# Performance work log

Measured on AMD Instinct MI355X. Metric: run time of the kernel, lower is better.

## Reference

```python
import jax, jax.numpy as jnp
import numpy as np

# ---- fixed wavelet filters (Selesnick FSfarras first-stage + Kingsbury Q-shift) ----
_F1 = np.array([
    [0.0, 0.0],
    [-0.08838834764832, -0.01122679215254],
    [0.08838834764832, 0.01122679215254],
    [0.69587998903400, 0.08838834764832],
    [0.69587998903400, 0.08838834764832],
    [0.08838834764832, -0.69587998903400],
    [-0.08838834764832, 0.69587998903400],
    [0.01122679215254, -0.08838834764832],
    [0.01122679215254, -0.08838834764832],
    [0.0, 0.0]], np.float32)
_F2 = np.array([
    [0.01122679215254, 0.0],
    [0.01122679215254, 0.0],
    [-0.08838834764832, -0.08838834764832],
    [0.08838834764832, -0.08838834764832],
    [0.69587998903400, 0.69587998903400],
    [0.69587998903400, -0.69587998903400],
    [0.08838834764832, 0.08838834764832],
    [-0.08838834764832, 0.08838834764832],
    [0.0, 0.01122679215254],
    [0.0, -0.01122679215254]], np.float32)
_Q1 = np.array([
    [0.03516384, 0.0],
    [0.0, 0.0],
    [-0.08832942, -0.11430184],
    [0.23389032, 0.0],
    [0.76027237, 0.58751830],
    [0.58751830, -0.76027237],
    [0.0, 0.23389032],
    [-0.11430184, 0.08832942],
    [0.0, 0.0],
    [0.0, -0.03516384]], np.float32)
_Q2 = np.array([
    [0.0, -0.03516384],
    [0.0, 0.0],
    [-0.11430184, 0.08832942],
    [0.0, 0.23389032],
    [0.58751830, -0.76027237],
    [0.76027237, 0.58751830],
    [0.23389032, 0.0],
    [-0.08832942, -0.11430184],
    [0.0, 0.0],
    [0.03516384, 0.0]], np.float32)
# synthesis filters are the time-reversed analysis filters
FSF = jnp.asarray(np.stack([_F1[::-1].copy(), _F2[::-1].copy()]))  # [2, 10, 2] first stage
SF = jnp.asarray(np.stack([_Q1[::-1].copy(), _Q2[::-1].copy()]))   # [2, 10, 2] Q-shift


def _upconv(x, f, axis):
    """Upsample-by-2 + full convolution with 1D filter f along `axis` (upfirdn(x,f,2,1))."""
    L = f.shape[0]
    xm = jnp.moveaxis(x, axis, -1)
    shp = xm.shape
    xr = xm.reshape(-1, 1, shp[-1])  # [M, 1, n] NCW
    k = f[::-1].astype(x.dtype).reshape(1, 1, L)  # flip -> true convolution
    y = jax.lax.conv_general_dilated(
        xr, k, window_strides=(1,), padding=[(L - 1, L - 1)],
        lhs_dilation=(2,), dimension_numbers=('NCW', 'OIW', 'NCW'))  # [M,1,2n+L-2]
    y = y.reshape(shp[:-1] + (y.shape[-1],))
    return jnp.moveaxis(y, -1, axis)


def sfb1d(lo, hi, sf, axis):
    """1D synthesis filter bank with periodic wrap + circular shift (Selesnick sfb1D)."""
    L = sf.shape[0]
    N = 2 * lo.shape[axis]
    y = _upconv(lo, sf[:, 0], axis) + _upconv(hi, sf[:, 1], axis)  # length N+L-2
    yN = jax.lax.slice_in_dim(y, 0, N, axis=axis)
    tail = jax.lax.slice_in_dim(y, N, N + L - 2, axis=axis)
    head = jax.lax.slice_in_dim(yN, 0, L - 2, axis=axis) + tail
    rest = jax.lax.slice_in_dim(yN, L - 2, N, axis=axis)
    return jnp.roll(jnp.concatenate([head, rest], axis=axis), 1 - L // 2, axis=axis)


def sfb2d(lo, hi3, sf_row, sf_col):
    """2D separable synthesis: hi3 = (LH, HL, HH); x is [B, H, W, C]."""
    lo = sfb1d(lo, hi3[0], sf_col, axis=2)
    h = sfb1d(hi3[1], hi3[2], sf_col, axis=2)
    return sfb1d(lo, h, sf_row, axis=1)


def _idtcwt(highs0, highs1, lows):
    inv_sqrt2 = jnp.asarray(1.0 / np.sqrt(2.0), highs0.dtype)

    def pm(a, b):
        return (a + b) * inv_sqrt2, (a - b) * inv_sqrt2

    # orientation butterflies per level (add_sub)
    wi = [[[[None] * 3 for _ in range(2)] for _ in range(2)] for _ in range(2)]
    for j, hj in enumerate((highs0, highs1)):
        for b in range(3):
            u, v = pm(hj[0, 0, b], hj[1, 1, b])
            wi[j][0][0][b], wi[j][1][1][b] = u, v
            u, v = pm(hj[0, 1, b], hj[1, 0, b])
            wi[j][0][1][b], wi[j][1][0][b] = u, v

    y = jnp.zeros_like(lows[0, 0], shape=(lows.shape[2], lows.shape[3] * 4,
                                          lows.shape[4] * 4, lows.shape[5]))
    for m in range(2):
        for n in range(2):
            lo = lows[m, n]
            lo = sfb2d(lo, wi[1][m][n], SF[m], SF[n])      # level 2 (Q-shift)
            lo = sfb2d(lo, wi[0][m][n], FSF[m], FSF[n])    # level 1 (first stage)
            y = y + lo
    return y / 2


def setup_inputs() -> dict:
    key = jax.random.key(0)
    k0, k1, k2 = jax.random.split(key, 3)
    B, C = 16, 3
    highs0 = jax.random.normal(k0, (2, 2, 3, B, 256, 256, C), dtype=jnp.float32)
    highs1 = jax.random.normal(k1, (2, 2, 3, B, 128, 128, C), dtype=jnp.float32)
    lows = jax.random.normal(k2, (2, 2, B, 128, 128, C), dtype=jnp.float32)
    return {"highs0": highs0, "highs1": highs1, "lows": lows}


def reference(highs0, highs1, lows):
    return _idtcwt(highs0, highs1, lows)
```

## Files before the change

### kernel.cpp

```cpp
#include <hip/hip_runtime.h>

#define INV_SQRT2 0.70710678118654752440f
#define KH 0.35355339059327376220f

constexpr float c_first[2][10][2] = {
  { { 0.00000000000000f,  0.00000000000000f},
    {-0.08838834764832f, -0.01122679215254f},
    { 0.08838834764832f,  0.01122679215254f},
    { 0.69587998903400f,  0.08838834764832f},
    { 0.69587998903400f,  0.08838834764832f},
    { 0.08838834764832f, -0.69587998903400f},
    {-0.08838834764832f,  0.69587998903400f},
    { 0.01122679215254f, -0.08838834764832f},
    { 0.01122679215254f, -0.08838834764832f},
    { 0.00000000000000f,  0.00000000000000f} },
  { { 0.01122679215254f,  0.00000000000000f},
    { 0.01122679215254f,  0.00000000000000f},
    {-0.08838834764832f, -0.08838834764832f},
    { 0.08838834764832f, -0.08838834764832f},
    { 0.69587998903400f,  0.69587998903400f},
    { 0.69587998903400f, -0.69587998903400f},
    { 0.08838834764832f,  0.08838834764832f},
    {-0.08838834764832f,  0.08838834764832f},
    { 0.00000000000000f,  0.01122679215254f},
    { 0.00000000000000f, -0.01122679215254f} }
};

constexpr float cq[2][10][2] = {
  { { 0.03516384f,  0.00000000f},
    { 0.00000000f,  0.00000000f},
    {-0.08832942f, -0.11430184f},
    { 0.23389032f,  0.00000000f},
    { 0.76027237f,  0.58751830f},
    { 0.58751830f, -0.76027237f},
    { 0.00000000f,  0.23389032f},
    {-0.11430184f,  0.08832942f},
    { 0.00000000f,  0.00000000f},
    { 0.00000000f, -0.03516384f} },
  { { 0.00000000f, -0.03516384f},
    { 0.00000000f,  0.00000000f},
    {-0.11430184f,  0.08832942f},
    { 0.00000000f,  0.23389032f},
    { 0.58751830f, -0.76027237f},
    { 0.76027237f,  0.58751830f},
    { 0.23389032f,  0.00000000f},
    {-0.08832942f, -0.11430184f},
    { 0.00000000f,  0.00000000f},
    { 0.03516384f,  0.00000000f} }
};

template<int M, int N>
__device__ __forceinline__ void s1_body(
    const float* __restrict__ lows, const float* __restrict__ highs1,
    float* __restrict__ lo2)
{
  constexpr int HIN = 128, WIN = 128, C = 3, B = 16;
  constexpr int ROWF  = WIN * C;
  constexpr int ROWO  = 2 * WIN * C;
  constexpr int PLANE = HIN * WIN * C;
  constexpr int SEG   = 16;
  constexpr int combo = M * 2 + N;
  constexpr int pa = (M == N) ? 0 : 1;
  constexpr int pb = (M == N) ? 3 : 2;
  constexpr float K = INV_SQRT2;

  const int jj = blockIdx.x * 128 + threadIdx.x;
  const int c  = jj % 3;
  const int t  = jj / 3;
  const int b  = blockIdx.z & 15;

  const float* lo = lows + (combo * B + b) * PLANE;
  const int bandStride = B * PLANE;
  const float* hA = highs1 + (pa * 3 * B + b) * PLANE;
  const float* hB = highs1 + (pb * 3 * B + b) * PLANE;

  int wc3[5];
#pragma unroll
  for (int p = 0; p < 5; ++p) {
    int w = t + 2 - p;
    if (w >= WIN) w -= WIN;
    if (w < 0)  w += WIN;
    wc3[p] = w * C + c;
  }

  float lae[5], lao[5], hae[5], hao[5];
#pragma unroll
  for (int k = 0; k < 5; ++k) { lae[k]=0.f; lao[k]=0.f; hae[k]=0.f; hao[k]=0.f; }

  const int s0 = blockIdx.y * SEG;
  float* outp = lo2 + (combo * B + b) * (4 * PLANE);

#pragma unroll 1
  for (int ui = 0; ui < SEG + 4; ++ui) {
    const int u  = (s0 - 2 + ui) & (HIN - 1);
#pragma unroll
    for (int k = 0; k < 4; ++k) { lae[k]=lae[k+1]; lao[k]=lao[k+1]; hae[k]=hae[k+1]; hao[k]=hao[k+1]; }
    const int rb = u * ROWF;

    float rl[5], rA[3][5], rB[3][5];
#pragma unroll
    for (int p = 0; p < 5; ++p) {
      const int idx = rb + wc3[p];
      rl[p]    = lo[idx];
      rA[0][p] = hA[idx];
      rB[0][p] = hB[idx];
      rA[1][p] = hA[idx +   bandStride];
      rB[1][p] = hB[idx +   bandStride];
      rA[2][p] = hA[idx + 2*bandStride];
      rB[2][p] = hB[idx + 2*bandStride];
    }
    asm volatile("" :: "v"(rl[0]),"v"(rl[1]),"v"(rl[2]),"v"(rl[3]),"v"(rl[4]),
                       "v"(rA[0][0]),"v"(rA[0][1]),"v"(rA[0][2]),"v"(rA[0][3]),"v"(rA[0][4]),
                       "v"(rA[1][0]),"v"(rA[1][1]),"v"(rA[1][2]),"v"(rA[1][3]),"v"(rA[1][4]));
    asm volatile("" :: "v"(rA[2][0]),"v"(rA[2][1]),"v"(rA[2][2]),"v"(rA[2][3]),"v"(rA[2][4]),
                       "v"(rB[0][0]),"v"(rB[0][1]),"v"(rB[0][2]),"v"(rB[0][3]),"v"(rB[0][4]),
                       "v"(rB[1][0]),"v"(rB[1][1]),"v"(rB[1][2]),"v"(rB[1][3]),"v"(rB[1][4]));
    asm volatile("" :: "v"(rB[2][0]),"v"(rB[2][1]),"v"(rB[2][2]),"v"(rB[2][3]),"v"(rB[2][4]));

    float aLe=0.f, aLo=0.f, aHe=0.f, aHo=0.f;
#pragma unroll
    for (int p = 0; p < 5; ++p) {
      const float lv  = rl[p];
      const float lhv = (M == 0) ? (rA[0][p] + rB[0][p]) : (rA[0][p] - rB[0][p]);
      const float hlv = (M == 0) ? (rA[1][p] + rB[1][p]) : (rA[1][p] - rB[1][p]);
      const float hhv = (M == 0) ? (rA[2][p] + rB[2][p]) : (rA[2][p] - rB[2][p]);
      const float ce0  = cq[N][9-2*p][0];
      const float co0  = cq[N][8-2*p][0];
      const float ce1K = cq[N][9-2*p][1] * K;
      const float co1K = cq[N][8-2*p][1] * K;
      const float ce0K = ce0 * K;
      const float co0K = co0 * K;
      aLe += ce0  * lv  + ce1K * lhv;
      aLo += co0  * lv  + co1K * lhv;
      aHe += ce0K * hlv + ce1K * hhv;
      aHo += co0K * hlv + co1K * hhv;
    }
    lae[4]=aLe; lao[4]=aLo; hae[4]=aHe; hao[4]=aHo;

    if (ui >= 4) {
      const int s = s0 + ui - 4;
      float o00=0.f, o01=0.f, o10=0.f, o11=0.f;
#pragma unroll
      for (int p = 0; p < 5; ++p) {
        const float f0l = cq[M][9-2*p][0], f0h = cq[M][9-2*p][1];
        const float f1l = cq[M][8-2*p][0], f1h = cq[M][8-2*p][1];
        o00 += f0l*lae[4-p] + f0h*hae[4-p];
        o01 += f0l*lao[4-p] + f0h*hao[4-p];
        o10 += f1l*lae[4-p] + f1h*hae[4-p];
        o11 += f1l*lao[4-p] + f1h*hao[4-p];
      }
      float* q = outp + (2*s) * ROWO + (2*t) * C + c;
      q[0]        = o00;
      q[C]        = o01;
      q[ROWO]     = o10;
      q[ROWO + C] = o11;
    }
  }
}

__global__ __launch_bounds__(128, 3) void idtcwt_stage1(
    const float* __restrict__ lows, const float* __restrict__ highs1,
    float* __restrict__ lo2)
{
  const int combo = blockIdx.z >> 4;
  if      (combo == 0) s1_body<0,0>(lows, highs1, lo2);
  else if (combo == 1) s1_body<0,1>(lows, highs1, lo2);
  else if (combo == 2) s1_body<1,0>(lows, highs1, lo2);
  else                 s1_body<1,1>(lows, highs1, lo2);
}

__global__ __launch_bounds__(256, 4) void idtcwt_stage2(
    const float* __restrict__ lo2, const float* __restrict__ highs0,
    float* __restrict__ out)
{
  constexpr int HIN = 256, WIN = 256, C = 3, B = 16;
  constexpr int ROWF  = WIN * C;
  constexpr int ROWO  = 2 * WIN * C;
  constexpr int PLANE = HIN * WIN * C;
  constexpr int OPLANE = 512 * 512 * C;
  constexpr int SEG   = 16;
  constexpr int NI    = SEG + 4;
  constexpr int PITCH = 5;
  constexpr int LDSV4 = 3072;

  __shared__ float4 lds4[LDSV4];

  const int tid = threadIdx.x;
  const int jj  = blockIdx.x * 256 + tid;
  const int c   = jj % 3;
  const int t   = jj / 3;
  const int b   = blockIdx.z;

  const int bandStride = B * PLANE;
  const float* a0  = lo2 + (0 * B + b) * PLANE;
  const float* a1  = lo2 + (1 * B + b) * PLANE;
  const float* a2  = lo2 + (2 * B + b) * PLANE;
  const float* a3  = lo2 + (3 * B + b) * PLANE;
  const float* h00b0 = highs0 + (0 * 3 * B + b) * PLANE;
  const float* h01b0 = highs0 + (1 * 3 * B + b) * PLANE;
  const float* h10b0 = highs0 + (2 * 3 * B + b) * PLANE;
  const float* h11b0 = highs0 + (3 * 3 * B + b) * PLANE;
  const float* h00b1 = h00b0 + bandStride;
  const float* h01b1 = h01b0 + bandStride;
  const float* h10b1 = h10b0 + bandStride;
  const float* h11b1 = h11b0 + bandStride;
  const float* h00b2 = h00b0 + 2*bandStride;
  const float* h01b2 = h01b0 + 2*bandStride;
  const float* h10b2 = h10b0 + 2*bandStride;
  const float* h11b2 = h11b0 + 2*bandStride;

  int j1 = jj - 6;   if (j1 < 0)     j1 += ROWF;
  int j2 = jj + 250; if (j2 >= ROWF) j2 -= ROWF;
  const bool halo = (tid < 12);

  float wla0e[5], wla0o[5], wla1e[5], wla1o[5];
  float wha0e[5], wha0o[5], wha1e[5], wha1o[5];
#pragma unroll
  for (int k = 0; k < 5; ++k) {
    wla0e[k]=0.f; wla0o[k]=0.f; wla1e[k]=0.f; wla1o[k]=0.f;
    wha0e[k]=0.f; wha0o[k]=0.f; wha1e[k]=0.f; wha1o[k]=0.f;
  }

  const int s0 = blockIdx.y * SEG;
  float* outb = out + b * OPLANE;

  float4 G0, G1, G2, G3;
  float4 Hh0 = make_float4(0.f,0.f,0.f,0.f), Hh1 = Hh0, Hh2 = Hh0, Hh3 = Hh0;

#define S2_LOAD(I)                                                           \
  {                                                                          \
    const int rb_ = ((s0 - 2 + (I)) & (HIN - 1)) * ROWF;                     \
    const int o1_ = rb_ + j1;                                                \
    G0 = make_float4(a0[o1_], a1[o1_], a2[o1_], a3[o1_]);                    \
    G1 = make_float4(h00b0[o1_], h11b0[o1_], h01b0[o1_], h10b0[o1_]);        \
    G2 = make_float4(h00b1[o1_], h11b1[o1_], h01b1[o1_], h10b1[o1_]);        \
    G3 = make_float4(h00b2[o1_], h11b2[o1_], h01b2[o1_], h10b2[o1_]);        \
    if (halo) {                                                              \
      const int o2_ = rb_ + j2;                                              \
      Hh0 = make_float4(a0[o2_], a1[o2_], a2[o2_], a3[o2_]);                 \
      Hh1 = make_float4(h00b0[o2_], h11b0[o2_], h01b0[o2_], h10b0[o2_]);     \
      Hh2 = make_float4(h00b1[o2_], h11b1[o2_], h01b1[o2_], h10b1[o2_]);     \
      Hh3 = make_float4(h00b2[o2_], h11b2[o2_], h01b2[o2_], h10b2[o2_]);     \
    }                                                                        \
  }

#define S2_WRITE()                                                           \
  {                                                                          \
    float4* w_ = lds4 + tid * PITCH;                                         \
    w_[0] = make_float4(G0.x*0.5f, G0.y*0.5f, G0.z*0.5f, G0.w*0.5f);         \
    w_[1] = make_float4((G1.x+G1.y)*KH, (G1.x-G1.y)*KH,                      \
                        (G1.z+G1.w)*KH, (G1.z-G1.w)*KH);                     \
    w_[2] = make_float4((G2.x+G2.y)*KH, (G2.x-G2.y)*KH,                      \
                        (G2.z+G2.w)*KH, (G2.z-G2.w)*KH);                     \
    w_[3] = make_float4((G3.x+G3.y)*KH, (G3.x-G3.y)*KH,                      \
                        (G3.z+G3.w)*KH, (G3.z-G3.w)*KH);                     \
    if (halo) {                                                              \
      float4* w2_ = lds4 + (256 + tid) * PITCH;                              \
      w2_[0] = make_float4(Hh0.x*0.5f, Hh0.y*0.5f, Hh0.z*0.5f, Hh0.w*0.5f);  \
      w2_[1] = make_float4((Hh1.x+Hh1.y)*KH, (Hh1.x-Hh1.y)*KH,               \
                           (Hh1.z+Hh1.w)*KH, (Hh1.z-Hh1.w)*KH);              \
      w2_[2] = make_float4((Hh2.x+Hh2.y)*KH, (Hh2.x-Hh2.y)*KH,               \
                           (Hh2.z+Hh2.w)*KH, (Hh2.z-Hh2.w)*KH);              \
      w2_[3] = make_float4((Hh3.x+Hh3.y)*KH, (Hh3.x-Hh3.y)*KH,               \
                           (Hh3.z+Hh3.w)*KH, (Hh3.z-Hh3.w)*KH);              \
    }                                                                        \
  }

  S2_LOAD(0);
  S2_WRITE();
  __syncthreads();

#pragma unroll 1
  for (int uo = 0; uo < 4; ++uo) {
#pragma unroll
    for (int k = 0; k < 5; ++k) {
      const int i = uo * 5 + k;

      if (i < NI - 1) {
        S2_LOAD(i + 1);
        __builtin_amdgcn_sched_barrier(0);
      }

      float A0e=0.f,A0o=0.f,A1e=0.f,A1o=0.f, H0e=0.f,H0o=0.f,H1e=0.f,H1o=0.f;
#pragma unroll
      for (int p = 0; p < 5; ++p) {
        const float4* qp = lds4 + (tid + (12 - 3*p)) * PITCH;
        const float4 q0 = qp[0], q1 = qp[1], q2 = qp[2], q3 = qp[3];
        const float a0e = c_first[0][9-2*p][0], a0o = c_first[0][8-2*p][0];
        const float b0e = c_first[0][9-2*p][1], b0o = c_first[0][8-2*p][1];
        const float a1e = c_first[1][9-2*p][0], a1o = c_first[1][8-2*p][0];
        const float b1e = c_first[1][9-2*p][1], b1o = c_first[1][8-2*p][1];
        A0e += a0e*q0.x + a1e*q0.y;   A0o += a0o*q0.x + a1o*q0.y;
        A1e += a0e*q0.z + a1e*q0.w;   A1o += a0o*q0.z + a1o*q0.w;
        A0e += b0e*q1.x + b1e*q1.z;   A0o += b0o*q1.x + b1o*q1.z;
        A1e += b0e*q1.w + b1e*q1.y;   A1o += b0o*q1.w + b1o*q1.y;
        H0e += a0e*q2.x + a1e*q2.z;   H0o += a0o*q2.x + a1o*q2.z;
        H1e += a0e*q2.w + a1e*q2.y;   H1o += a0o*q2.w + a1o*q2.y;
        H0e += b0e*q3.x + b1e*q3.z;   H0o += b0o*q3.x + b1o*q3.z;
        H1e += b0e*q3.w + b1e*q3.y;   H1o += b0o*q3.w + b1o*q3.y;
      }
      wla0e[k]=A0e; wla0o[k]=A0o; wla1e[k]=A1e; wla1o[k]=A1o;
      wha0e[k]=H0e; wha0o[k]=H0o; wha1e[k]=H1e; wha1o[k]=H1o;

      if (i >= 4) {
        const int s = s0 + i - 4;
        float o00=0.f, o01=0.f, o10=0.f, o11=0.f;
#pragma unroll
        for (int p = 0; p < 5; ++p) {
          const int kk = (k - p + 5) % 5;
          const float f00 = c_first[0][9-2*p][0], g00 = c_first[0][9-2*p][1];
          const float f01 = c_first[0][8-2*p][0], g01 = c_first[0][8-2*p][1];
          const float f10 = c_first[1][9-2*p][0], g10 = c_first[1][9-2*p][1];
          const float f11 = c_first[1][8-2*p][0], g11 = c_first[1][8-2*p][1];
          o00 += f00*wla0e[kk] + g00*wha0e[kk] + f10*wla1e[kk] + g10*wha1e[kk];
          o01 += f00*wla0o[kk] + g00*wha0o[kk] + f10*wla1o[kk] + g10*wha1o[kk];
          o10 += f01*wla0e[kk] + g01*wha0e[kk] + f11*wla1e[kk] + g11*wha1e[kk];
          o11 += f01*wla0o[kk] + g01*wha0o[kk] + f11*wla1o[kk] + g11*wha1o[kk];
        }
        float* q = outb + (2*s) * ROWO + (2*t) * C + c;
        q[0]        = o00;
        q[C]        = o01;
        q[ROWO]     = o10;
        q[ROWO + C] = o11;
      }

      __syncthreads();
      if (i < NI - 1) {
        S2_WRITE();
      }
      __syncthreads();
    }
  }
#undef S2_LOAD
#undef S2_WRITE
}

extern "C" void kernel_launch(void* const* d_in, const int* in_sizes, int n_in,
                              void* d_out, int out_size, void* d_ws, size_t ws_size,
                              hipStream_t stream) {
  const float* highs0 = (const float*)d_in[0];
  const float* highs1 = (const float*)d_in[1];
  const float* lows   = (const float*)d_in[2];
  float* out = (float*)d_out;
  float* lo2 = (float*)d_ws;

  dim3 b1(128), g1(3, 8, 64);
  hipLaunchKernelGGL(idtcwt_stage1, g1, b1, 0, stream, lows, highs1, lo2);

  dim3 b2(256), g2(3, 16, 16);
  hipLaunchKernelGGL(idtcwt_stage2, g2, b2, 0, stream, lo2, highs0, out);
}
```

Before: 107.9 us.

## Stage input rows in LDS for stage1 horizontal filter with prefetch pipelining

Stage1 previously had each thread load 5 horizontal taps from global memory for each of 7 arrays, 35 loads per row. Now each thread loads one element per array (plus a 12-element halo for the first 12 threads), applies the butterfly, and writes the combined 4 rows into LDS. The 5-tap horizontal filter then reads neighbours from LDS. The next row's global loads are issued before the current row's compute to overlap latency. This cuts redundant global and L1 traffic, at the cost of two __syncthreads per row and some LDS usage.

```diff
diff --git a/kernel.cpp b/kernel.cpp
--- a/kernel.cpp
+++ b/kernel.cpp
@@ -52,36 +52,34 @@
 template<int M, int N>
 __device__ __forceinline__ void s1_body(
     const float* __restrict__ lows, const float* __restrict__ highs1,
-    float* __restrict__ lo2)
+    float* __restrict__ lo2, float* __restrict__ lds)
 {
   constexpr int HIN = 128, WIN = 128, C = 3, B = 16;
   constexpr int ROWF  = WIN * C;
   constexpr int ROWO  = 2 * WIN * C;
   constexpr int PLANE = HIN * WIN * C;
   constexpr int SEG   = 16;
+  constexpr int NI    = SEG + 4;
+  constexpr int PITCH = 144;
   constexpr int combo = M * 2 + N;
   constexpr int pa = (M == N) ? 0 : 1;
   constexpr int pb = (M == N) ? 3 : 2;
   constexpr float K = INV_SQRT2;
 
-  const int jj = blockIdx.x * 128 + threadIdx.x;
-  const int c  = jj % 3;
-  const int t  = jj / 3;
-  const int b  = blockIdx.z & 15;
+  const int tid = threadIdx.x;
+  const int jj  = blockIdx.x * 128 + tid;
+  const int c   = jj % 3;
+  const int t   = jj / 3;
+  const int b   = blockIdx.z & 15;
 
   const float* lo = lows + (combo * B + b) * PLANE;
   const int bandStride = B * PLANE;
   const float* hA = highs1 + (pa * 3 * B + b) * PLANE;
   const float* hB = highs1 + (pb * 3 * B + b) * PLANE;
 
-  int wc3[5];
-#pragma unroll
-  for (int p = 0; p < 5; ++p) {
-    int w = t + 2 - p;
-    if (w >= WIN) w -= WIN;
-    if (w < 0)  w += WIN;
-    wc3[p] = w * C + c;
-  }
+  int j1 = jj - 6;   if (j1 < 0)     j1 += ROWF;
+  int j2 = jj + 122; if (j2 >= ROWF) j2 -= ROWF;
+  const bool halo = (tid < 12);
 
   float lae[5], lao[5], hae[5], hao[5];
 #pragma unroll
@@ -90,83 +88,119 @@
   const int s0 = blockIdx.y * SEG;
   float* outp = lo2 + (combo * B + b) * (4 * PLANE);
 
+  float rl, rA0, rB0, rA1, rB1, rA2, rB2;
+  float hl = 0.f, hA0v = 0.f, hB0v = 0.f, hA1v = 0.f,
+        hB1v = 0.f, hA2v = 0.f, hB2v = 0.f;
+
+#define BFY(a_, b_) ((M == 0) ? ((a_) + (b_)) : ((a_) - (b_)))
+
+#define S1_LOAD(I)                                                           \
+  {                                                                          \
+    const int rb_ = ((s0 - 2 + (I)) & (HIN - 1)) * ROWF;                     \
+    rl  = lo[rb_ + j1];                                                      \
+    rA0 = hA[rb_ + j1];                rB0 = hB[rb_ + j1];                   \
+    rA1 = hA[rb_ + j1 + bandStride];   rB1 = hB[rb_ + j1 + bandStride];      \
+    rA2 = hA[rb_ + j1 + 2*bandStride]; rB2 = hB[rb_ + j1 + 2*bandStride];    \
+    if (halo) {                                                              \
+      hl   = lo[rb_ + j2];                                                   \
+      hA0v = hA[rb_ + j2];                hB0v = hB[rb_ + j2];               \
+      hA1v = hA[rb_ + j2 + bandStride];   hB1v = hB[rb_ + j2 + bandStride];  \
+      hA2v = hA[rb_ + j2 + 2*bandStride]; hB2v = hB[rb_ + j2 + 2*bandStride];\
+    }                                                                        \
+  }
+
+#define S1_WRITE()                                                           \
+  {                                                                          \
+    lds[0*PITCH + tid] = rl;                                                 \
+    lds[1*PITCH + tid] = BFY(rA0, rB0);                                      \
+    lds[2*PITCH + tid] = BFY(rA1, rB1);                                      \
+    lds[3*PITCH + tid] = BFY(rA2, rB2);                                      \
+    if (halo) {                                                              \
+      lds[0*PITCH + 128 + tid] = hl;                                         \
+      lds[1*PITCH + 128 + tid] = BFY(hA0v, hB0v);                            \
+      lds[2*PITCH + 128 + tid] = BFY(hA1v, hB1v);                            \
+      lds[3*PITCH + 128 + tid] = BFY(hA2v, hB2v);                            \
+    }                                                                        \
+  }
+
+  S1_LOAD(0);
+  S1_WRITE();
+  __syncthreads();
+
 #pragma unroll 1
-  for (int ui = 0; ui < SEG + 4; ++ui) {
-    const int u  = (s0 - 2 + ui) & (HIN - 1);
-#pragma unroll
-    for (int k = 0; k < 4; ++k) { lae[k]=lae[k+1]; lao[k]=lao[k+1]; hae[k]=hae[k+1]; hao[k]=hao[k+1]; }
-    const int rb = u * ROWF;
-
-    float rl[5], rA[3][5], rB[3][5];
-#pragma unroll
-    for (int p = 0; p < 5; ++p) {
-      const int idx = rb + wc3[p];
-      rl[p]    = lo[idx];
-      rA[0][p] = hA[idx];
-      rB[0][p] = hB[idx];
-      rA[1][p] = hA[idx +   bandStride];
-      rB[1][p] = hB[idx +   bandStride];
-      rA[2][p] = hA[idx + 2*bandStride];
-      rB[2][p] = hB[idx + 2*bandStride];
+  for (int uo = 0; uo < 4; ++uo) {
+#pragma unroll
+    for (int k = 0; k < 5; ++k) {
+      const int i = uo * 5 + k;
+
+      if (i < NI - 1) {
+        S1_LOAD(i + 1);
+        __builtin_amdgcn_sched_barrier(0);
+      }
+
+      float aLe=0.f, aLo=0.f, aHe=0.f, aHo=0.f;
+#pragma unroll
+      for (int p = 0; p < 5; ++p) {
+        const int sl = tid + (12 - 3*p);
+        const float lv  = lds[0*PITCH + sl];
+        const float lhv = lds[1*PITCH + sl];
+        const float hlv = lds[2*PITCH + sl];
+        const float hhv = lds[3*PITCH + sl];
+        const float ce0  = cq[N][9-2*p][0];
+        const float co0  = cq[N][8-2*p][0];
+        const float ce1K = cq[N][9-2*p][1] * K;
+        const float co1K = cq[N][8-2*p][1] * K;
+        const float ce0K = ce0 * K;
+        const float co0K = co0 * K;
+        aLe += ce0  * lv  + ce1K * lhv;
+        aLo += co0  * lv  + co1K * lhv;
+        aHe += ce0K * hlv + ce1K * hhv;
+        aHo += co0K * hlv + co1K * hhv;
+      }
+      lae[k]=aLe; lao[k]=aLo; hae[k]=aHe; hao[k]=aHo;
+
+      if (i >= 4) {
+        const int s = s0 + i - 4;
+        float o00=0.f, o01=0.f, o10=0.f, o11=0.f;
+#pragma unroll
+        for (int p = 0; p < 5; ++p) {
+          const int kk = (k - p + 5) % 5;
+          const float f0l = cq[M][9-2*p][0], f0h = cq[M][9-2*p][1];
+          const float f1l = cq[M][8-2*p][0], f1h = cq[M][8-2*p][1];
+          o00 += f0l*lae[kk] + f0h*hae[kk];
+          o01 += f0l*lao[kk] + f0h*hao[kk];
+          o10 += f1l*lae[kk] + f1h*hae[kk];
+          o11 += f1l*lao[kk] + f1h*hao[kk];
+        }
+        float* q = outp + (2*s) * ROWO + (2*t) * C + c;
+        q[0]        = o00;
+        q[C]        = o01;
+        q[ROWO]     = o10;
+        q[ROWO + C] = o11;
+      }
+
+      __syncthreads();
+      if (i < NI - 1) {
+        S1_WRITE();
+      }
+      __syncthreads();
     }
-    asm volatile("" :: "v"(rl[0]),"v"(rl[1]),"v"(rl[2]),"v"(rl[3]),"v"(rl[4]),
-                       "v"(rA[0][0]),"v"(rA[0][1]),"v"(rA[0][2]),"v"(rA[0][3]),"v"(rA[0][4]),
-                       "v"(rA[1][0]),"v"(rA[1][1]),"v"(rA[1][2]),"v"(rA[1][3]),"v"(rA[1][4]));
-    asm volatile("" :: "v"(rA[2][0]),"v"(rA[2][1]),"v"(rA[2][2]),"v"(rA[2][3]),"v"(rA[2][4]),
-                       "v"(rB[0][0]),"v"(rB[0][1]),"v"(rB[0][2]),"v"(rB[0][3]),"v"(rB[0][4]),
-                       "v"(rB[1][0]),"v"(rB[1][1]),"v"(rB[1][2]),"v"(rB[1][3]),"v"(rB[1][4]));
-    asm volatile("" :: "v"(rB[2][0]),"v"(rB[2][1]),"v"(rB[2][2]),"v"(rB[2][3]),"v"(rB[2][4]));
-
-    float aLe=0.f, aLo=0.f, aHe=0.f, aHo=0.f;
-#pragma unroll
-    for (int p = 0; p < 5; ++p) {
-      const float lv  = rl[p];
-      const float lhv = (M == 0) ? (rA[0][p] + rB[0][p]) : (rA[0][p] - rB[0][p]);
-      const float hlv = (M == 0) ? (rA[1][p] + rB[1][p]) : (rA[1][p] - rB[1][p]);
-      const float hhv = (M == 0) ? (rA[2][p] + rB[2][p]) : (rA[2][p] - rB[2][p]);
-      const float ce0  = cq[N][9-2*p][0];
-      const float co0  = cq[N][8-2*p][0];
-      const float ce1K = cq[N][9-2*p][1] * K;
-      const float co1K = cq[N][8-2*p][1] * K;
-      const float ce0K = ce0 * K;
-      const float co0K = co0 * K;
-      aLe += ce0  * lv  + ce1K * lhv;
-      aLo += co0  * lv  + co1K * lhv;
-      aHe += ce0K * hlv + ce1K * hhv;
-      aHo += co0K * hlv + co1K * hhv;
-    }
-    lae[4]=aLe; lao[4]=aLo; hae[4]=aHe; hao[4]=aHo;
-
-    if (ui >= 4) {
-      const int s = s0 + ui - 4;
-      float o00=0.f, o01=0.f, o10=0.f, o11=0.f;
-#pragma unroll
-      for (int p = 0; p < 5; ++p) {
-        const float f0l = cq[M][9-2*p][0], f0h = cq[M][9-2*p][1];
-        const float f1l = cq[M][8-2*p][0], f1h = cq[M][8-2*p][1];
-        o00 += f0l*lae[4-p] + f0h*hae[4-p];
-        o01 += f0l*lao[4-p] + f0h*hao[4-p];
-        o10 += f1l*lae[4-p] + f1h*hae[4-p];
-        o11 += f1l*lao[4-p] + f1h*hao[4-p];
-      }
-      float* q = outp + (2*s) * ROWO + (2*t) * C + c;
-      q[0]        = o00;
-      q[C]        = o01;
-      q[ROWO]     = o10;
-      q[ROWO + C] = o11;
-    }
-  }
+  }
+#undef S1_LOAD
+#undef S1_WRITE
+#undef BFY
 }
 
 __global__ __launch_bounds__(128, 3) void idtcwt_stage1(
     const float* __restrict__ lows, const float* __restrict__ highs1,
     float* __restrict__ lo2)
 {
+  __shared__ float s1lds[6800];
   const int combo = blockIdx.z >> 4;
-  if      (combo == 0) s1_body<0,0>(lows, highs1, lo2);
-  else if (combo == 1) s1_body<0,1>(lows, highs1, lo2);
-  else if (combo == 2) s1_body<1,0>(lows, highs1, lo2);
-  else                 s1_body<1,1>(lows, highs1, lo2);
+  if      (combo == 0) s1_body<0,0>(lows, highs1, lo2, s1lds);
+  else if (combo == 1) s1_body<0,1>(lows, highs1, lo2, s1lds);
+  else if (combo == 2) s1_body<1,0>(lows, highs1, lo2, s1lds);
+  else                 s1_body<1,1>(lows, highs1, lo2, s1lds);
 }
 
 __global__ __launch_bounds__(256, 4) void idtcwt_stage2(
```

Measured after the change: 105.1 us, median of 2. 2.6% less time.
